# Optimization experiments

Measured on AMD Instinct MI355X. Metric: run time of the kernel, lower is better.

## Reference

```python
import jax, jax.numpy as jnp
import numpy as np

B, S, D, H = 4, 1024, 768, 12
DH = D // H            # 64
MAXPOS = 1024          # config.max_position_embeddings
NTYPES = 8             # flow types (embedding has NTYPES+1 rows, row 0 = padding)


def setup_inputs() -> dict:
    key = jax.random.key(0)
    ks = jax.random.split(key, 12)
    sc = 0.02
    inp = {
        "hidden_states": jax.random.normal(ks[0], (B, S, D), jnp.float32),
        "Wq": jax.random.normal(ks[1], (D, D), jnp.float32) * sc,
        "bq": jnp.zeros((D,), jnp.float32),
        "Wk": jax.random.normal(ks[2], (D, D), jnp.float32) * sc,
        "bk": jnp.zeros((D,), jnp.float32),
        "Wv": jax.random.normal(ks[3], (D, D), jnp.float32) * sc,
        "bv": jnp.zeros((D,), jnp.float32),
        "dist_emb": jax.random.normal(ks[4], (2 * MAXPOS - 1, DH), jnp.float32) * sc,
        "cfg_emb": jax.random.normal(ks[5], (NTYPES + 1, 1), jnp.float32) * sc,
        "dfg_emb": jax.random.normal(ks[6], (NTYPES + 1, 1), jnp.float32) * sc,
        "rfg_emb": jax.random.normal(ks[7], (NTYPES + 1, 1), jnp.float32) * sc,
        "cfg_matrix": jax.random.randint(ks[8], (B, S, S), 0, NTYPES + 1, jnp.int32),
        "dfg_matrix": jax.random.randint(ks[9], (B, S, S), 0, NTYPES + 1, jnp.int32),
        "rdg_matrix": jax.random.randint(ks[10], (B, S, S), 0, NTYPES + 1, jnp.int32),
    }
    return inp


def reference(hidden_states, Wq, bq, Wk, bk, Wv, bv, dist_emb,
              cfg_emb, dfg_emb, rfg_emb, cfg_matrix, dfg_matrix, rdg_matrix):
    b, s, d = hidden_states.shape
    inv_sqrt = 1.0 / float(np.sqrt(DH))

    def heads(x):  # [b,s,d] -> [b,H,s,DH]
        return x.reshape(b, s, H, DH).transpose(0, 2, 1, 3)

    q = heads(hidden_states @ Wq.T + bq)
    k = heads(hidden_states @ Wk.T + bk)
    v = heads(hidden_states @ Wv.T + bv)

    scores = jnp.einsum('bhld,bhrd->bhlr', q, k)

    # relative_key_query positional bias
    dist = jnp.arange(s)[:, None] - jnp.arange(s)[None, :] + (MAXPOS - 1)
    pe = dist_emb[dist]  # [s, s, DH]
    scores = scores + jnp.einsum('bhld,lrd->bhlr', q, pe) \
                    + jnp.einsum('bhrd,lrd->bhlr', k, pe)

    scores = scores * inv_sqrt

    # flow-type bias: scalar embedding per (i,j), padding row 0 forced to zero
    flow = (cfg_emb.at[0].set(0.0)[cfg_matrix][..., 0]
            + dfg_emb.at[0].set(0.0)[dfg_matrix][..., 0]
            + rfg_emb.at[0].set(0.0)[rdg_matrix][..., 0])  # [b,s,s]
    scores = scores + flow[:, None, :, :]

    probs = jax.nn.softmax(scores, axis=-1)
    ctx = jnp.einsum('bhlr,bhrd->bhld', probs, v)
    return ctx.transpose(0, 2, 1, 3).reshape(b, s, d)
```

## Files before the change

kernel.cpp:

```cpp
#include <hip/hip_runtime.h>


typedef __attribute__((ext_vector_type(4))) float f32x4;
typedef __attribute__((ext_vector_type(8))) short s16x8;

#define MFMA_BF16 __builtin_amdgcn_mfma_f32_16x16x32_bf16
#define SQRT_C 0.42466086f

__device__ __forceinline__ unsigned short f2bf(float x) {
  unsigned u = __builtin_bit_cast(unsigned, x);
  u += 0x7fffu + ((u >> 16) & 1u);
  return (unsigned short)(u >> 16);
}
__device__ __forceinline__ float bf2f(unsigned short h) {
  unsigned u = ((unsigned)h) << 16;
  return __builtin_bit_cast(float, u);
}
__device__ __forceinline__ float exp2_fast(float x) {
  float r;
  asm("v_exp_f32 %0, %1" : "=v"(r) : "v"(x));
  return r;
}
__device__ __forceinline__ void gl_lds16(const void* g, void* l) {
  __builtin_amdgcn_global_load_lds(
      (const __attribute__((address_space(1))) unsigned int*)g,
      (__attribute__((address_space(3))) unsigned int*)l, 16, 0, 0);
}

__global__ __launch_bounds__(256) void k_prep(
    const float* __restrict__ hs, const float* __restrict__ wq,
    const float* __restrict__ wk, const float* __restrict__ wv,
    const float* __restrict__ de, unsigned short* __restrict__ hsb,
    unsigned short* __restrict__ wb, unsigned short* __restrict__ db) {
  const long HSN = 3145728, WN = 1769472;
  long e = ((long)blockIdx.x * 256 + threadIdx.x) * 4;
  if (e < HSN) {
    float4 v = *(const float4*)(hs + e);
    *(ushort4*)(hsb + e) = make_ushort4(f2bf(v.x), f2bf(v.y), f2bf(v.z), f2bf(v.w));
  } else if (e < HSN + WN) {
    long ew = e - HSN;
    const float* src = (ew >= 1179648) ? wv : ((ew >= 589824) ? wk : wq);
    long off = (ew >= 1179648) ? (ew - 1179648) : ((ew >= 589824) ? (ew - 589824) : ew);
    float4 v = *(const float4*)(src + off);
    *(ushort4*)(wb + ew) = make_ushort4(f2bf(v.x), f2bf(v.y), f2bf(v.z), f2bf(v.w));
  } else {
    long ed = e - HSN - WN;
    ushort4 ov;
    if (ed < 131008) {
      float4 v = *(const float4*)(de + ed);
      ov = make_ushort4(f2bf(v.x * SQRT_C), f2bf(v.y * SQRT_C),
                        f2bf(v.z * SQRT_C), f2bf(v.w * SQRT_C));
    } else {
      ov = make_ushort4(0, 0, 0, 0);
    }
    *(ushort4*)(db + ed) = ov;
  }
}

__global__ __launch_bounds__(256) void k_flow(
    const int* __restrict__ cm, const int* __restrict__ dm,
    const int* __restrict__ rm, const float* __restrict__ ce,
    const float* __restrict__ dfe, const float* __restrict__ rfe,
    unsigned short* __restrict__ flT) {
  const int tid = threadIdx.x;
  const int rt = blockIdx.x, lt = blockIdx.y, b = blockIdx.z;
  const int l15 = tid & 15, g = (tid >> 4) & 3, w = tid >> 6;
  const int rowb = lt * 64 + w * 16 + g * 4;
  const int colb = rt * 64 + l15;
  s16x8 o0, o1;
#pragma unroll
  for (int n = 0; n < 4; ++n) {
#pragma unroll
    for (int r = 0; r < 4; ++r) {
      const long idx = ((long)b << 20) + ((long)(rowb + r) << 10) + colb + (n << 4);
      const int c = cm[idx], d = dm[idx], rr = rm[idx];
      const float v = (c ? ce[c] : 0.f) + (d ? dfe[d] : 0.f) + (rr ? rfe[rr] : 0.f);
      const short hv = (short)f2bf(1.4426950408889634f * v);
      if (n < 2) o0[n * 4 + r] = hv; else o1[(n - 2) * 4 + r] = hv;
    }
  }
  unsigned short* dst =
      flT + ((long)((((b << 4) + lt) << 4) | rt) << 12) + (tid << 4);
  *(s16x8*)(dst) = o0;
  *(s16x8*)(dst + 8) = o1;
}

__global__ __launch_bounds__(256) void k_qkv(
    const unsigned short* __restrict__ A, const unsigned short* __restrict__ W,
    const float* __restrict__ bq, const float* __restrict__ bk,
    const float* __restrict__ bv, unsigned short* __restrict__ Qp,
    unsigned short* __restrict__ Kp, unsigned short* __restrict__ Vp) {
  __shared__ __align__(16) char smq[16384];
  char* sa = smq;
  char* sb = smq + 8192;
  const int tid = threadIdx.x, w = tid >> 6, lane = tid & 63;
  const int g = lane >> 4, l15 = lane & 15;
  const int n0 = blockIdx.x * 128, m0 = blockIdx.y * 128;
  const int wm = w >> 1, wn = w & 1;
  f32x4 acc[4][4] = {};
  for (int k0 = 0; k0 < 768; k0 += 32) {
#pragma unroll
    for (int it = 0; it < 2; ++it) {
      const int c = (w << 7) + (it << 6) + lane;
      const int row = c >> 2, sl = c & 3;
      const int so = ((sl ^ ((row >> 1) & 3)) << 3);
      char* dst = smq + ((w << 7) + (it << 6)) * 16;
      gl_lds16(A + (long)(m0 + row) * 768 + k0 + so, dst);
      gl_lds16(W + (long)(n0 + row) * 768 + k0 + so, dst + 8192);
    }
    __syncthreads();
    s16x8 af[4], bf[4];
#pragma unroll
    for (int mi = 0; mi < 4; ++mi) {
      const int row = wm * 64 + mi * 16 + l15;
      af[mi] = *(const s16x8*)(sa + row * 64 + ((g ^ ((row >> 1) & 3)) << 4));
    }
#pragma unroll
    for (int ni = 0; ni < 4; ++ni) {
      const int row = wn * 64 + ni * 16 + l15;
      bf[ni] = *(const s16x8*)(sb + row * 64 + ((g ^ ((row >> 1) & 3)) << 4));
    }
#pragma unroll
    for (int mi = 0; mi < 4; ++mi)
#pragma unroll
      for (int ni = 0; ni < 4; ++ni)
        acc[mi][ni] = MFMA_BF16(af[mi], bf[ni], acc[mi][ni], 0, 0, 0);
    __syncthreads();
  }
  const int t_sel = n0 / 768;
  const float* bias = (t_sel == 0) ? bq : (t_sel == 1) ? bk : bv;
  unsigned short* dst = (t_sel == 0) ? Qp : (t_sel == 1) ? Kp : Vp;
  const float osc = (t_sel == 2) ? 1.0f : SQRT_C;
#pragma unroll
  for (int ni = 0; ni < 4; ++ni) {
    const int mcol = n0 + wn * 64 + ni * 16 + l15;
    const int nw2 = mcol - t_sel * 768;
    const float bvv = bias[nw2];
    const int h = nw2 >> 6, dh = nw2 & 63;
#pragma unroll
    for (int mi = 0; mi < 4; ++mi) {
#pragma unroll
      for (int r = 0; r < 4; ++r) {
        const int token = m0 + wm * 64 + mi * 16 + (g << 2) + r;
        const int b = token >> 10, s = token & 1023;
        const long idx = ((((long)(b * 12 + h)) << 10) + s) * 64 + dh;
        dst[idx] = f2bf((acc[mi][ni][r] + bvv) * osc);
      }
    }
  }
}

__global__ __launch_bounds__(256) void k_vt(const unsigned short* __restrict__ Vp,
                                            unsigned short* __restrict__ Vt) {
  __shared__ __align__(16) unsigned short t[64][64];
  const int bh = blockIdx.y, s0 = blockIdx.x * 64;
  const int tid = threadIdx.x;
#pragma unroll
  for (int it = 0; it < 2; ++it) {
    const int c = it * 256 + tid;
    const int row = c >> 3, sl = c & 7;
    const int slot = sl ^ ((row >> 3) & 7);
    s16x8 v = *(const s16x8*)(Vp + (((long)bh << 10) + s0 + row) * 64 + sl * 8);
    *(s16x8*)&t[row][slot * 8] = v;
  }
  __syncthreads();
#pragma unroll
  for (int it = 0; it < 2; ++it) {
    const int c = it * 256 + tid;
    const int d = c >> 3, ss = c & 7;
    const int cg = d >> 3;
    s16x8 vv;
#pragma unroll
    for (int i = 0; i < 8; ++i) {
      const int rr = ss * 8 + i;
      vv[i] = (short)t[rr][((cg ^ ((rr >> 3) & 7)) << 3) + (d & 7)];
    }
    *(s16x8*)(Vt + (((long)bh * 64 + d) << 10) + s0 + ss * 8) = vv;
  }
}

__global__ __launch_bounds__(256, 3) void k_attn(
    const unsigned short* __restrict__ Qp, const unsigned short* __restrict__ Kp,
    const unsigned short* __restrict__ Vtp, const unsigned short* __restrict__ Db,
    const unsigned short* __restrict__ FlT, float* __restrict__ Out) {
  __shared__ __align__(16) char sm[50688];
  char* Kl = sm;
  char* Vl = sm + 8192;
  char* Dl = sm + 16384;
  unsigned short* KDs = (unsigned short*)(sm + 32768);
  char* Pl = sm + 41472;

  const int tid = threadIdx.x, w = tid >> 6, lane = tid & 63;
  const int g = lane >> 4, l15 = lane & 15;
  const int l0 = blockIdx.x << 6, h = blockIdx.y, b = blockIdx.z;
  const int bh = b * 12 + h;
  const unsigned short* Qb = Qp + ((long)bh << 16);
  const unsigned short* Kb = Kp + ((long)bh << 16);
  const unsigned short* Vb = Vtp + ((long)bh << 16);
  const unsigned short* fTb =
      FlT + ((long)(((b << 4) + blockIdx.x) << 4) << 12) + (tid << 4);

  const int qrow = l0 + (w << 4) + l15;
  const s16x8 qf0 = *(const s16x8*)(Qb + (long)qrow * 64 + g * 8);
  const s16x8 qf1 = *(const s16x8*)(Qb + (long)qrow * 64 + 32 + g * 8);

  int srcad[4];
  bool msk[4];
#pragma unroll
  for (int r = 0; r < 4; ++r) {
    const int bl = ((g << 2) + r - 1) & 15;
    srcad[r] = (((lane & 48) + ((bl - l15) & 15)) << 2);
    msk[r] = (l15 <= bl);
  }
  const bool g0 = (g == 0);

  f32x4 oacc[4] = {};
  float lpart[4] = {0.f, 0.f, 0.f, 0.f};

  for (int rt = 0; rt < 16; ++rt) {
    const int r0 = rt << 6;
    const int t0 = l0 - r0 + 960;

    const s16x8 fv0 = *(const s16x8*)(fTb + ((long)rt << 12));
    const s16x8 fv1 = *(const s16x8*)(fTb + ((long)rt << 12) + 8);

#pragma unroll
    for (int it = 0; it < 2; ++it) {
      const int c = (w << 7) + (it << 6) + lane;
      const int row = c >> 3, sl = c & 7;
      const int so = ((sl ^ (row & 7)) << 3);
      char* dst = sm + ((w << 7) + (it << 6)) * 16;
      gl_lds16(Kb + (long)(r0 + row) * 64 + so, dst);
      gl_lds16(Vb + (long)row * 1024 + r0 + so, dst + 8192);
    }
    {
      const int nh = (rt == 0) ? 2 : 1;
      for (int hh = 0; hh < nh; ++hh) {
        const int ts = t0 + (hh << 6);
        char* dhalf = Dl + (((ts >> 6) & 1) << 13);
#pragma unroll
        for (int it = 0; it < 2; ++it) {
          const int c = (w << 7) + (it << 6) + lane;
          const int row = c >> 3, sl = c & 7;
          gl_lds16(Db + (long)(ts + row) * 64 + ((sl ^ (row & 7)) << 3),
                   dhalf + ((w << 7) + (it << 6)) * 16);
        }
      }
    }
    __syncthreads();

    __builtin_amdgcn_s_setprio(1);
    f32x4 qa[5];
#pragma unroll
    for (int lt = 0; lt < 5; ++lt) {
      const int nq = w + lt;
      const int pb = ((((t0 >> 6) + (nq >> 2)) & 1) << 6) + ((nq & 3) << 4);
      const int trow = pb + l15;
      const s16x8 d0 = *(const s16x8*)(Dl + trow * 128 + ((g ^ (trow & 7)) << 4));
      const s16x8 d1 = *(const s16x8*)(Dl + trow * 128 + (((4 + g) ^ (trow & 7)) << 4));
      f32x4 a = {};
      a = MFMA_BF16(qf0, d0, a, 0, 0, 0);
      a = MFMA_BF16(qf1, d1, a, 0, 0, 0);
      qa[lt] = a;
    }

    {
      const int krow = (w << 4) + l15;
      const s16x8 kf0 = *(const s16x8*)(Kl + krow * 128 + ((g ^ (krow & 7)) << 4));
      const s16x8 kf1 = *(const s16x8*)(Kl + krow * 128 + (((4 + g) ^ (krow & 7)) << 4));
#pragma unroll
      for (int kt = 0; kt < 5; ++kt) {
        const int nk = 3 - w + kt;
        const int pb = ((((t0 >> 6) + (nk >> 2)) & 1) << 6) + ((nk & 3) << 4);
        const int trow = pb + l15;
        const s16x8 d0 = *(const s16x8*)(Dl + trow * 128 + ((g ^ (trow & 7)) << 4));
        const s16x8 d1 = *(const s16x8*)(Dl + trow * 128 + (((4 + g) ^ (trow & 7)) << 4));
        f32x4 ka = {};
        ka = MFMA_BF16(kf0, d0, ka, 0, 0, 0);
        ka = MFMA_BF16(kf1, d1, ka, 0, 0, 0);
#pragma unroll
        for (int r = 0; r < 4; ++r) {
          const int prow = (w << 4) + (g << 2) + r;
          const int ck = (kt << 4) + l15 + (g << 2) + r - 15;
          if (kt == 0 || kt == 4) {
            if ((unsigned)ck < 64u) KDs[prow * 68 + ck] = f2bf(ka[r]);
          } else {
            KDs[prow * 68 + ck] = f2bf(ka[r]);
          }
        }
      }
    }
    __builtin_amdgcn_s_setprio(0);
    __syncthreads();

    __builtin_amdgcn_s_setprio(1);
    f32x4 sacc[4] = {};
#pragma unroll
    for (int n = 0; n < 4; ++n) {
      const int kr = (n << 4) + l15;
      const s16x8 b0 = *(const s16x8*)(Kl + kr * 128 + ((g ^ (kr & 7)) << 4));
      const s16x8 b1 = *(const s16x8*)(Kl + kr * 128 + (((4 + g) ^ (kr & 7)) << 4));
      sacc[n] = MFMA_BF16(qf0, b0, sacc[n], 0, 0, 0);
      sacc[n] = MFMA_BF16(qf1, b1, sacc[n], 0, 0, 0);
    }
    __builtin_amdgcn_s_setprio(0);
#pragma unroll
    for (int n = 0; n < 4; ++n) {
      const int j = (n << 4) + l15;
      const uint2 kdp =
          *(const uint2*)(KDs + j * 68 + (w << 4) + (g << 2));
#pragma unroll
      for (int r = 0; r < 4; ++r) {
        float hi, lo;
        if (r == 0) {
          hi = g0 ? qa[3 - n][0] : qa[4 - n][0];
          lo = qa[3 - n][0];
        } else {
          hi = qa[4 - n][r];
          lo = qa[3 - n][r];
        }
        const float vsrc = msk[r] ? hi : lo;
        const float qd = __builtin_bit_cast(
            float, __builtin_amdgcn_ds_bpermute(
                       srcad[r], __builtin_bit_cast(int, vsrc)));
        const unsigned kdw = (r < 2) ? kdp.x : kdp.y;
        const float kd = bf2f((unsigned short)(kdw >> ((r & 1) << 4)));
        const float fv = bf2f((unsigned short)(
            n < 2 ? fv0[(n << 2) + r] : fv1[((n - 2) << 2) + r]));
        sacc[n][r] = sacc[n][r] + qd + kd + fv;
      }
    }

#pragma unroll
    for (int r = 0; r < 4; ++r) {
      const float p0 = exp2_fast(sacc[0][r]);
      const float p1 = exp2_fast(sacc[1][r]);
      const float p2 = exp2_fast(sacc[2][r]);
      const float p3 = exp2_fast(sacc[3][r]);
      sacc[0][r] = p0; sacc[1][r] = p1; sacc[2][r] = p2; sacc[3][r] = p3;
      lpart[r] += (p0 + p1) + (p2 + p3);
    }

#pragma unroll
    for (int n = 0; n < 4; ++n) {
#pragma unroll
      for (int r = 0; r < 4; ++r) {
        const int ib = (w << 4) + (g << 2) + r;
        const int j = (n << 4) + l15;
        *(unsigned short*)(Pl + ib * 144 + (((j >> 3) ^ (ib & 7)) << 4) +
                           ((j & 7) << 1)) = f2bf(sacc[n][r]);
      }
    }

    __builtin_amdgcn_s_setprio(1);
#pragma unroll
    for (int k0 = 0; k0 < 2; ++k0) {
      const int prow = (w << 4) + l15;
      const s16x8 pf = *(const s16x8*)(
          Pl + prow * 144 + ((((k0 << 2) + g) ^ (prow & 7)) << 4));
#pragma unroll
      for (int n = 0; n < 4; ++n) {
        const int vrow = (n << 4) + l15;
        const s16x8 vf = *(const s16x8*)(
            Vl + vrow * 128 + ((((k0 << 2) + g) ^ (vrow & 7)) << 4));
        oacc[n] = MFMA_BF16(pf, vf, oacc[n], 0, 0, 0);
      }
    }
    __builtin_amdgcn_s_setprio(0);
    __syncthreads();
  }

  float lsum[4];
#pragma unroll
  for (int r = 0; r < 4; ++r) {
    float s = lpart[r];
#pragma unroll
    for (int dd = 1; dd < 16; dd <<= 1) s += __shfl_xor(s, dd, 64);
    lsum[r] = s;
  }
#pragma unroll
  for (int n = 0; n < 4; ++n) {
#pragma unroll
    for (int r = 0; r < 4; ++r) {
      const int l = l0 + (w << 4) + (g << 2) + r;
      const int d = (n << 4) + l15;
      Out[((long)(b * 1024 + l)) * 768 + h * 64 + d] = oacc[n][r] / lsum[r];
    }
  }
}

extern "C" void kernel_launch(void* const* d_in, const int* in_sizes, int n_in,
                              void* d_out, int out_size, void* d_ws, size_t ws_size,
                              hipStream_t stream) {
  const float* hs = (const float*)d_in[0];
  const float* Wq = (const float*)d_in[1];
  const float* bq = (const float*)d_in[2];
  const float* Wk = (const float*)d_in[3];
  const float* bk = (const float*)d_in[4];
  const float* Wv = (const float*)d_in[5];
  const float* bv = (const float*)d_in[6];
  const float* de = (const float*)d_in[7];
  const float* ce = (const float*)d_in[8];
  const float* dfe = (const float*)d_in[9];
  const float* rfe = (const float*)d_in[10];
  const int* cm = (const int*)d_in[11];
  const int* dm = (const int*)d_in[12];
  const int* rm = (const int*)d_in[13];
  float* out = (float*)d_out;
  char* ws = (char*)d_ws;

  unsigned short* hsb = (unsigned short*)(ws + 0);
  unsigned short* wb  = (unsigned short*)(ws + 6291456);
  unsigned short* db  = (unsigned short*)(ws + 9830400);
  unsigned short* flT = (unsigned short*)(ws + 10092544);
  unsigned short* qp  = (unsigned short*)(ws + 18481152);
  unsigned short* kp  = (unsigned short*)(ws + 24772608);
  unsigned short* vp  = (unsigned short*)(ws + 31064064);
  unsigned short* vt  = (unsigned short*)(ws + 37355520);

  k_prep<<<4928, 256, 0, stream>>>(hs, Wq, Wk, Wv, de, hsb, wb, db);
  k_flow<<<dim3(16, 16, 4), 256, 0, stream>>>(cm, dm, rm, ce, dfe, rfe, flT);
  k_qkv<<<dim3(18, 32), 256, 0, stream>>>(hsb, wb, bq, bk, bv, qp, kp, vp);
  k_vt<<<dim3(16, 48), 256, 0, stream>>>(vp, vt);
  k_attn<<<dim3(16, 12, 4), 256, 0, stream>>>(qp, kp, vt, db, flT, out);
}
```

Measured before the change: 112.4 us.

## Fuse flow-bias, QKV GEMM and V transpose into one launch

Merges the flow-bias kernel into the QKV projection launch as extra blocks (ids 576+), so the memory-bound flow gather can overlap the compute-bound GEMM. It also writes V directly in transposed layout through an LDS staging tile in the GEMM epilogue, which removes the separate transpose kernel and the intermediate V buffer round trip. This cuts two kernel launches. The cost is heavier shared memory use and extra syncs in the V-block epilogue.

```diff
diff --git a/kernel.cpp b/kernel.cpp
--- a/kernel.cpp
+++ b/kernel.cpp
@@ -57,45 +57,52 @@
   }
 }
 
-__global__ __launch_bounds__(256) void k_flow(
+__global__ __launch_bounds__(256) void k_qkvf(
+    const unsigned short* __restrict__ A, const unsigned short* __restrict__ W,
+    const float* __restrict__ bq, const float* __restrict__ bk,
+    const float* __restrict__ bv, unsigned short* __restrict__ Qp,
+    unsigned short* __restrict__ Kp, unsigned short* __restrict__ Vt,
     const int* __restrict__ cm, const int* __restrict__ dm,
     const int* __restrict__ rm, const float* __restrict__ ce,
     const float* __restrict__ dfe, const float* __restrict__ rfe,
     unsigned short* __restrict__ flT) {
+  __shared__ __align__(16) char smq[18432];
   const int tid = threadIdx.x;
-  const int rt = blockIdx.x, lt = blockIdx.y, b = blockIdx.z;
-  const int l15 = tid & 15, g = (tid >> 4) & 3, w = tid >> 6;
-  const int rowb = lt * 64 + w * 16 + g * 4;
-  const int colb = rt * 64 + l15;
-  s16x8 o0, o1;
-#pragma unroll
-  for (int n = 0; n < 4; ++n) {
-#pragma unroll
-    for (int r = 0; r < 4; ++r) {
-      const long idx = ((long)b << 20) + ((long)(rowb + r) << 10) + colb + (n << 4);
-      const int c = cm[idx], d = dm[idx], rr = rm[idx];
-      const float v = (c ? ce[c] : 0.f) + (d ? dfe[d] : 0.f) + (rr ? rfe[rr] : 0.f);
-      const short hv = (short)f2bf(1.4426950408889634f * v);
-      if (n < 2) o0[n * 4 + r] = hv; else o1[(n - 2) * 4 + r] = hv;
-    }
-  }
-  unsigned short* dst =
-      flT + ((long)((((b << 4) + lt) << 4) | rt) << 12) + (tid << 4);
-  *(s16x8*)(dst) = o0;
-  *(s16x8*)(dst + 8) = o1;
-}
-
-__global__ __launch_bounds__(256) void k_qkv(
-    const unsigned short* __restrict__ A, const unsigned short* __restrict__ W,
-    const float* __restrict__ bq, const float* __restrict__ bk,
-    const float* __restrict__ bv, unsigned short* __restrict__ Qp,
-    unsigned short* __restrict__ Kp, unsigned short* __restrict__ Vp) {
-  __shared__ __align__(16) char smq[16384];
+  const int id = blockIdx.x;
+
+  if (id >= 576) {
+    const int fid = id - 576;
+    const int rt = fid & 15, lt = (fid >> 4) & 15, b = fid >> 8;
+    const int l15 = tid & 15, g = (tid >> 4) & 3, w = tid >> 6;
+    const int rowb = lt * 64 + w * 16 + g * 4;
+    const int colb = rt * 64 + l15;
+    s16x8 o0, o1;
+#pragma unroll
+    for (int n = 0; n < 4; ++n) {
+#pragma unroll
+      for (int r = 0; r < 4; ++r) {
+        const long idx =
+            ((long)b << 20) + ((long)(rowb + r) << 10) + colb + (n << 4);
+        const int c = cm[idx], d = dm[idx], rr = rm[idx];
+        const float v =
+            (c ? ce[c] : 0.f) + (d ? dfe[d] : 0.f) + (rr ? rfe[rr] : 0.f);
+        const short hv = (short)f2bf(1.4426950408889634f * v);
+        if (n < 2) o0[n * 4 + r] = hv; else o1[(n - 2) * 4 + r] = hv;
+      }
+    }
+    unsigned short* dst =
+        flT + ((long)((((b << 4) + lt) << 4) | rt) << 12) + (tid << 4);
+    *(s16x8*)(dst) = o0;
+    *(s16x8*)(dst + 8) = o1;
+    return;
+  }
+
   char* sa = smq;
   char* sb = smq + 8192;
-  const int tid = threadIdx.x, w = tid >> 6, lane = tid & 63;
+  const int w = tid >> 6, lane = tid & 63;
   const int g = lane >> 4, l15 = lane & 15;
-  const int n0 = blockIdx.x * 128, m0 = blockIdx.y * 128;
+  const int bx = id % 18, by = id / 18;
+  const int n0 = bx * 128, m0 = by * 128;
   const int wm = w >> 1, wn = w & 1;
   f32x4 acc[4][4] = {};
   for (int k0 = 0; k0 < 768; k0 += 32) {
@@ -128,54 +135,60 @@
     __syncthreads();
   }
   const int t_sel = n0 / 768;
-  const float* bias = (t_sel == 0) ? bq : (t_sel == 1) ? bk : bv;
-  unsigned short* dst = (t_sel == 0) ? Qp : (t_sel == 1) ? Kp : Vp;
-  const float osc = (t_sel == 2) ? 1.0f : SQRT_C;
-#pragma unroll
-  for (int ni = 0; ni < 4; ++ni) {
-    const int mcol = n0 + wn * 64 + ni * 16 + l15;
-    const int nw2 = mcol - t_sel * 768;
-    const float bvv = bias[nw2];
-    const int h = nw2 >> 6, dh = nw2 & 63;
-#pragma unroll
-    for (int mi = 0; mi < 4; ++mi) {
-#pragma unroll
-      for (int r = 0; r < 4; ++r) {
-        const int token = m0 + wm * 64 + mi * 16 + (g << 2) + r;
-        const int b = token >> 10, s = token & 1023;
-        const long idx = ((((long)(b * 12 + h)) << 10) + s) * 64 + dh;
-        dst[idx] = f2bf((acc[mi][ni][r] + bvv) * osc);
-      }
-    }
-  }
-}
-
-__global__ __launch_bounds__(256) void k_vt(const unsigned short* __restrict__ Vp,
-                                            unsigned short* __restrict__ Vt) {
-  __shared__ __align__(16) unsigned short t[64][64];
-  const int bh = blockIdx.y, s0 = blockIdx.x * 64;
-  const int tid = threadIdx.x;
-#pragma unroll
-  for (int it = 0; it < 2; ++it) {
-    const int c = it * 256 + tid;
-    const int row = c >> 3, sl = c & 7;
-    const int slot = sl ^ ((row >> 3) & 7);
-    s16x8 v = *(const s16x8*)(Vp + (((long)bh << 10) + s0 + row) * 64 + sl * 8);
-    *(s16x8*)&t[row][slot * 8] = v;
-  }
-  __syncthreads();
-#pragma unroll
-  for (int it = 0; it < 2; ++it) {
-    const int c = it * 256 + tid;
-    const int d = c >> 3, ss = c & 7;
-    const int cg = d >> 3;
-    s16x8 vv;
-#pragma unroll
-    for (int i = 0; i < 8; ++i) {
-      const int rr = ss * 8 + i;
-      vv[i] = (short)t[rr][((cg ^ ((rr >> 3) & 7)) << 3) + (d & 7)];
-    }
-    *(s16x8*)(Vt + (((long)bh * 64 + d) << 10) + s0 + ss * 8) = vv;
+  if (t_sel < 2) {
+    const float* bias = (t_sel == 0) ? bq : bk;
+    unsigned short* dst = (t_sel == 0) ? Qp : Kp;
+#pragma unroll
+    for (int ni = 0; ni < 4; ++ni) {
+      const int mcol = n0 + wn * 64 + ni * 16 + l15;
+      const int nw2 = mcol - t_sel * 768;
+      const float bvv = bias[nw2];
+      const int h = nw2 >> 6, dh = nw2 & 63;
+#pragma unroll
+      for (int mi = 0; mi < 4; ++mi) {
+#pragma unroll
+        for (int r = 0; r < 4; ++r) {
+          const int token = m0 + wm * 64 + mi * 16 + (g << 2) + r;
+          const int b = token >> 10, s = token & 1023;
+          const long idx = ((((long)(b * 12 + h)) << 10) + s) * 64 + dh;
+          dst[idx] = f2bf((acc[mi][ni][r] + bvv) * SQRT_C);
+        }
+      }
+    }
+  } else {
+    const int nv0 = n0 - 1536;
+    const int b = m0 >> 10, s0 = m0 & 1023;
+    unsigned short* tv = (unsigned short*)smq;
+    const int dh = tid >> 2, seg = tid & 3;
+#pragma unroll
+    for (int hh = 0; hh < 2; ++hh) {
+      if (wn == hh) {
+#pragma unroll
+        for (int ni = 0; ni < 4; ++ni) {
+          const int colh = ni * 16 + l15;
+          const float bvv = bv[nv0 + hh * 64 + colh];
+#pragma unroll
+          for (int mi = 0; mi < 4; ++mi)
+#pragma unroll
+            for (int r = 0; r < 4; ++r)
+              tv[(wm * 64 + mi * 16 + (g << 2) + r) * 72 + colh] =
+                  f2bf(acc[mi][ni][r] + bvv);
+        }
+      }
+      __syncthreads();
+      const int hB = (nv0 >> 6) + hh;
+      unsigned short* vrow =
+          Vt + ((long)((b * 12 + hB) * 64 + dh) << 10) + s0;
+#pragma unroll
+      for (int q = 0; q < 4; ++q) {
+        s16x8 vv;
+#pragma unroll
+        for (int i = 0; i < 8; ++i)
+          vv[i] = (short)tv[(seg * 32 + q * 8 + i) * 72 + dh];
+        *(s16x8*)(vrow + seg * 32 + q * 8) = vv;
+      }
+      __syncthreads();
+    }
   }
 }
 
@@ -415,12 +428,10 @@
   unsigned short* flT = (unsigned short*)(ws + 10092544);
   unsigned short* qp  = (unsigned short*)(ws + 18481152);
   unsigned short* kp  = (unsigned short*)(ws + 24772608);
-  unsigned short* vp  = (unsigned short*)(ws + 31064064);
   unsigned short* vt  = (unsigned short*)(ws + 37355520);
 
   k_prep<<<4928, 256, 0, stream>>>(hs, Wq, Wk, Wv, de, hsb, wb, db);
-  k_flow<<<dim3(16, 16, 4), 256, 0, stream>>>(cm, dm, rm, ce, dfe, rfe, flT);
-  k_qkv<<<dim3(18, 32), 256, 0, stream>>>(hsb, wb, bq, bk, bv, qp, kp, vp);
-  k_vt<<<dim3(16, 48), 256, 0, stream>>>(vp, vt);
+  k_qkvf<<<1600, 256, 0, stream>>>(hsb, wb, bq, bk, bv, qp, kp, vt,
+                                   cm, dm, rm, ce, dfe, rfe, flT);
   k_attn<<<dim3(16, 12, 4), 256, 0, stream>>>(qp, kp, vt, db, flT, out);
 }
```

After: 111.2 us. No clear change (-1.1%).
